# Kernel tuning notes

Measured on AMD Instinct MI355X. Metric: run time of the kernel, lower is better.

The kernel has to match this reference:

```python
import jax, jax.numpy as jnp
import numpy as np
import math

B, T, C = 32, 256, 1024
LAYER_ID, NUM_LAYERS = 12, 24
NEG_INF = -1e38


def setup_inputs() -> dict:
    key = jax.random.key(0)
    ks = jax.random.split(key, 5)
    x = jax.random.normal(ks[0], (B, T, C), dtype=jnp.float32)
    # deterministic parameter init, faithful to the torch __init__
    r01 = LAYER_ID / (NUM_LAYERS - 1)          # ratio_0_to_1
    r10 = 1.0 - LAYER_ID / NUM_LAYERS          # ratio_1_to_almost0
    h = jnp.arange(C, dtype=jnp.float32)
    time_decay = -5.0 + 8.0 * (h / (C - 1)) ** (0.7 + 1.3 * r01)
    tf = (jnp.arange(C) + 1) % 3 - 1
    time_first = jnp.full((C,), math.log(0.3), jnp.float32) + 0.5 * tf.astype(jnp.float32)
    xr = (jnp.arange(C, dtype=jnp.float32) / C)[None, None, :]   # [1,1,C]
    time_mix_k = xr ** r10
    time_mix_v = xr ** r10 + 0.3 * r01
    time_mix_r = xr ** (0.5 * r10)
    s = 1.0 / math.sqrt(C)
    Wk = jax.random.normal(ks[1], (C, C), jnp.float32) * s
    Wv = jax.random.normal(ks[2], (C, C), jnp.float32) * s
    Wr = jax.random.normal(ks[3], (C, C), jnp.float32) * s
    Wo = jax.random.normal(ks[4], (C, C), jnp.float32) * s
    return {"x": x, "time_decay": time_decay, "time_first": time_first,
            "time_mix_k": time_mix_k, "time_mix_v": time_mix_v, "time_mix_r": time_mix_r,
            "Wk": Wk, "Wv": Wv, "Wr": Wr, "Wo": Wo}


def wkv(time_decay, time_first, k, v):
    """Numerically-stabilized WKV scan. k,v: [B,T,C]; decay/first: [C]."""
    w = -jnp.exp(time_decay)   # per-channel log-decay (negative)
    u = time_first
    kT = jnp.swapaxes(k, 0, 1)  # [T,B,C]
    vT = jnp.swapaxes(v, 0, 1)

    def step(carry, kv):
        p, q, o = carry                       # p,q: running num/den; o: log scale
        kt, vt = kv                           # [B,C]
        no = jnp.maximum(o, u + kt)
        A = jnp.exp(o - no)
        Bc = jnp.exp(u + kt - no)
        y = (A * p + Bc * vt) / (A * q + Bc)
        no2 = jnp.maximum(w + o, kt)
        A2 = jnp.exp(w + o - no2)
        B2 = jnp.exp(kt - no2)
        return (A2 * p + B2 * vt, A2 * q + B2, no2), y

    init = (jnp.zeros((k.shape[0], k.shape[2]), k.dtype),
            jnp.zeros((k.shape[0], k.shape[2]), k.dtype),
            jnp.full((k.shape[0], k.shape[2]), NEG_INF, k.dtype))
    _, yT = jax.lax.scan(step, init, (kT, vT))
    return jnp.swapaxes(yT, 0, 1)  # [B,T,C]


def reference(x, time_decay, time_first, time_mix_k, time_mix_v, time_mix_r, Wk, Wv, Wr, Wo):
    # time_shift: xx[t] = x[t-1], xx[0] = 0
    xx = jnp.pad(x, ((0, 0), (1, 0), (0, 0)))[:, :-1, :]
    xk = x * time_mix_k + xx * (1.0 - time_mix_k)
    xv = x * time_mix_v + xx * (1.0 - time_mix_v)
    xr = x * time_mix_r + xx * (1.0 - time_mix_r)
    k = jnp.einsum('btc,dc->btd', xk, Wk)
    v = jnp.einsum('btc,dc->btd', xv, Wv)
    r = jnp.einsum('btc,dc->btd', xr, Wr)
    sr = jax.nn.sigmoid(r)
    rwkv = sr * wkv(time_decay, time_first, k, v)
    return jnp.einsum('btc,dc->btd', rwkv, Wo)
```

## Files before the change

### kernel.cpp

```cpp
#include <hip/hip_runtime.h>

#define Bdim 32
#define Tdim 256
#define Cdim 1024
#define Mrows (Bdim * Tdim)

typedef unsigned short u16;
typedef unsigned int u32;
typedef __bf16 bf16x8 __attribute__((ext_vector_type(8)));
typedef float f32x4 __attribute__((ext_vector_type(4)));

__device__ __forceinline__ float bf2f(u32 u) {
    union { u32 i; float f; } v; v.i = u << 16; return v.f;
}
__device__ __forceinline__ u16 f2bf(float f) {
    union { float f; u32 i; } v; v.f = f;
    u32 u = v.i;
    return (u16)((u + 0x7fffu + ((u >> 16) & 1u)) >> 16);
}

__device__ __forceinline__ void gload16(const u16* g, u16* l) {
    __builtin_amdgcn_global_load_lds(
        (__attribute__((address_space(1))) const void*)g,
        (__attribute__((address_space(3))) void*)l, 16, 0, 0);
}

__global__ __launch_bounds__(256) void prep_fused(
    const float* __restrict__ x, const float* __restrict__ tmk,
    const float* __restrict__ tmv, const float* __restrict__ tmr,
    u16* __restrict__ xk, u16* __restrict__ xv, u16* __restrict__ xr,
    const float* __restrict__ w0, const float* __restrict__ w1,
    const float* __restrict__ w2, const float* __restrict__ w3,
    u16* __restrict__ o0, u16* __restrict__ o1,
    u16* __restrict__ o2, u16* __restrict__ o3)
{
    int bid = blockIdx.x;
    if (bid < 4096) {
        int tid = bid * 256 + threadIdx.x;
        int e = tid << 3;
        int c = e & (Cdim - 1);
        int t = (e >> 10) & (Tdim - 1);
        float xf[8], xxf[8], mk[8], mv[8], mr[8];
        *(float4*)(xf)     = *(const float4*)(x + e);
        *(float4*)(xf + 4) = *(const float4*)(x + e + 4);
        if (t != 0) {
            *(float4*)(xxf)     = *(const float4*)(x + e - Cdim);
            *(float4*)(xxf + 4) = *(const float4*)(x + e - Cdim + 4);
        } else {
#pragma unroll
            for (int j = 0; j < 8; j++) xxf[j] = 0.f;
        }
        *(float4*)(mk)     = *(const float4*)(tmk + c);
        *(float4*)(mk + 4) = *(const float4*)(tmk + c + 4);
        *(float4*)(mv)     = *(const float4*)(tmv + c);
        *(float4*)(mv + 4) = *(const float4*)(tmv + c + 4);
        *(float4*)(mr)     = *(const float4*)(tmr + c);
        *(float4*)(mr + 4) = *(const float4*)(tmr + c + 4);
        u16 ok[8], ov[8], orr[8];
#pragma unroll
        for (int j = 0; j < 8; j++) {
            float d = xf[j] - xxf[j];
            ok[j]  = f2bf(xxf[j] + d * mk[j]);
            ov[j]  = f2bf(xxf[j] + d * mv[j]);
            orr[j] = f2bf(xxf[j] + d * mr[j]);
        }
        *(uint4*)(xk + e) = *(const uint4*)ok;
        *(uint4*)(xv + e) = *(const uint4*)ov;
        *(uint4*)(xr + e) = *(const uint4*)orr;
    } else {
        int wb = bid - 4096;
        int m = wb >> 9;
        const float* src; u16* dst;
        switch (m) {
            case 0: src = w0; dst = o0; break;
            case 1: src = w1; dst = o1; break;
            case 2: src = w2; dst = o2; break;
            default: src = w3; dst = o3; break;
        }
        int i = (((wb & 511) << 8) + threadIdx.x) << 3;
        float a[8];
        *(float4*)(a)     = *(const float4*)(src + i);
        *(float4*)(a + 4) = *(const float4*)(src + i + 4);
        u16 o[8];
#pragma unroll
        for (int j = 0; j < 8; j++) o[j] = f2bf(a[j]);
        *(uint4*)(dst + i) = *(const uint4*)o;
    }
}

template <int BF16OUT>
__device__ __forceinline__ void gemm_body(
    const u16* __restrict__ A, const u16* __restrict__ Bw, void* __restrict__ Cout,
    u16* As0, u16* Bs0, u16* As1, u16* Bs1, int bm, int bn)
{
    const int K = Cdim, N = Cdim;
    const int tid = threadIdx.x;
    const int lane = tid & 63, wave = tid >> 6;
    const int wm = (wave & 1) << 6, wn = (wave >> 1) << 6;
    const int fr = lane & 15, quad = lane >> 4;

    const int srow = tid >> 2;
    const int skc = (tid & 3) << 3;
    const u16* ga = A + (size_t)(bm * 128 + srow) * K + skc;
    const u16* gb = Bw + (size_t)(bn * 128 + srow) * K + skc;
    u16* la0 = As0 + (wave << 9);
    u16* lb0 = Bs0 + (wave << 9);
    u16* la1 = As1 + (wave << 9);
    u16* lb1 = Bs1 + (wave << 9);
    const size_t gstep = (size_t)64 * K;

    f32x4 acc[4][4];
#pragma unroll
    for (int i = 0; i < 4; i++)
#pragma unroll
        for (int j = 0; j < 4; j++)
            acc[i][j] = (f32x4){0.f, 0.f, 0.f, 0.f};

    for (int k0 = 0; k0 < K; k0 += 64) {
        __syncthreads();
        gload16(ga, la0);
        gload16(ga + gstep, la0 + 2048);
        gload16(gb, lb0);
        gload16(gb + gstep, lb0 + 2048);
        gload16(ga + 32, la1);
        gload16(ga + 32 + gstep, la1 + 2048);
        gload16(gb + 32, lb1);
        gload16(gb + 32 + gstep, lb1 + 2048);
        ga += 64; gb += 64;
        __syncthreads();
#pragma unroll
        for (int h = 0; h < 2; h++) {
            const u16* Ah = h ? As1 : As0;
            const u16* Bh = h ? Bs1 : Bs0;
            bf16x8 af[4], bfr[4];
#pragma unroll
            for (int i = 0; i < 4; i++) {
                af[i]  = *(const bf16x8*)(Ah + (wm + i * 16 + fr) * 32 + quad * 8);
                bfr[i] = *(const bf16x8*)(Bh + (wn + i * 16 + fr) * 32 + quad * 8);
            }
#pragma unroll
            for (int i = 0; i < 4; i++)
#pragma unroll
                for (int j = 0; j < 4; j++)
                    acc[i][j] = __builtin_amdgcn_mfma_f32_16x16x32_bf16(
                        af[i], bfr[j], acc[i][j], 0, 0, 0);
        }
    }

    const int gr0 = bm * 128 + wm + quad * 4;
    const int gc0 = bn * 128 + wn + fr;
#pragma unroll
    for (int i = 0; i < 4; i++)
#pragma unroll
        for (int j = 0; j < 4; j++)
#pragma unroll
            for (int r = 0; r < 4; r++) {
                int gr = gr0 + i * 16 + r;
                int gc = gc0 + j * 16;
                float val = acc[i][j][r];
                if (BF16OUT)
                    ((u16*)Cout)[(size_t)gr * N + gc] = f2bf(val);
                else
                    ((float*)Cout)[(size_t)gr * N + gc] = val;
            }
}

__global__ __launch_bounds__(256) void gemm3_kernel(
    const u16* __restrict__ xk, const u16* __restrict__ xv, const u16* __restrict__ xr,
    const u16* __restrict__ wk, const u16* __restrict__ wv, const u16* __restrict__ wr,
    u16* __restrict__ ck, u16* __restrict__ cv, u16* __restrict__ cr)
{
    __shared__ u16 As0[128 * 32], Bs0[128 * 32], As1[128 * 32], Bs1[128 * 32];
    const u16* A; const u16* Bw; u16* Cout;
    switch (blockIdx.z) {
        case 0:  A = xk; Bw = wk; Cout = ck; break;
        case 1:  A = xv; Bw = wv; Cout = cv; break;
        default: A = xr; Bw = wr; Cout = cr; break;
    }
    int bx = blockIdx.x;
    gemm_body<1>(A, Bw, (void*)Cout, As0, Bs0, As1, Bs1, bx & 63, bx >> 6);
}

__global__ __launch_bounds__(256) void gemmo_kernel(
    const u16* __restrict__ A, const u16* __restrict__ Bw, float* __restrict__ Cout)
{
    __shared__ u16 As0[128 * 32], Bs0[128 * 32], As1[128 * 32], Bs1[128 * 32];
    int bx = blockIdx.x;
    gemm_body<0>(A, Bw, (void*)Cout, As0, Bs0, As1, Bs1, bx & 63, bx >> 6);
}

#define WTC 16

#define LOADCHUNK(KA, VA, RA, T0)                                        \
    _Pragma("unroll")                                                    \
    for (int s = 0; s < WTC; s++) {                                      \
        size_t idx = base + (size_t)((T0) + s) * Cdim;                   \
        KA[s] = kb[idx]; VA[s] = vb[idx]; RA[s] = rb[idx];               \
    }

#define COMPCHUNK(KA, VA, RA, T0)                                        \
    _Pragma("unroll")                                                    \
    for (int s = 0; s < WTC; s++) {                                      \
        float kt = bf2f(KA[s]);                                          \
        float vt = bf2f(VA[s]);                                          \
        float rt = bf2f(RA[s]);                                          \
        float uk = u + kt;                                               \
        float no = fmaxf(o, uk);                                         \
        float Ae = __expf(o - no);                                       \
        float Bc = __expf(uk - no);                                      \
        float num = Ae * p + Bc * vt;                                    \
        float den = Ae * q + Bc;                                         \
        float y = num * __builtin_amdgcn_rcpf(den);                      \
        float sr = __builtin_amdgcn_rcpf(1.f + __expf(-rt));             \
        rwkv[base + (size_t)((T0) + s) * Cdim] = f2bf(y * sr);           \
        float wo = w + o;                                                \
        float no2 = fmaxf(wo, kt);                                       \
        float A2 = __expf(wo - no2);                                     \
        float B2 = __expf(kt - no2);                                     \
        p = A2 * p + B2 * vt;                                            \
        q = A2 * q + B2;                                                 \
        o = no2;                                                         \
    }

__global__ __launch_bounds__(64) void wkv_kernel(
    const u16* __restrict__ kb, const u16* __restrict__ vb,
    const u16* __restrict__ rb, const float* __restrict__ td,
    const float* __restrict__ tfirst, u16* __restrict__ rwkv)
{
    int lane = threadIdx.x;
    int blk = blockIdx.x;
    int b = blk >> 4;
    int c = ((blk & 15) << 6) + lane;
    float w = -__expf(td[c]);
    float u = tfirst[c];
    const size_t base = (size_t)b * Tdim * Cdim + c;

    u32 kA[WTC], vA[WTC], rA[WTC];
    u32 kB[WTC], vB[WTC], rB[WTC];
    float p = 0.f, q = 0.f, o = -1e38f;

    LOADCHUNK(kA, vA, rA, 0)
    for (int t0 = 0; t0 < Tdim; t0 += 2 * WTC) {
        LOADCHUNK(kB, vB, rB, t0 + WTC)
        COMPCHUNK(kA, vA, rA, t0)
        if (t0 + 2 * WTC < Tdim) {
            LOADCHUNK(kA, vA, rA, t0 + 2 * WTC)
        }
        COMPCHUNK(kB, vB, rB, t0 + WTC)
    }
}

extern "C" void kernel_launch(void* const* d_in, const int* in_sizes, int n_in,
                              void* d_out, int out_size, void* d_ws, size_t ws_size,
                              hipStream_t stream) {
    (void)in_sizes; (void)n_in; (void)out_size; (void)ws_size;
    const float* x   = (const float*)d_in[0];
    const float* td  = (const float*)d_in[1];
    const float* tfi = (const float*)d_in[2];
    const float* tmk = (const float*)d_in[3];
    const float* tmv = (const float*)d_in[4];
    const float* tmr = (const float*)d_in[5];
    const float* Wk  = (const float*)d_in[6];
    const float* Wv  = (const float*)d_in[7];
    const float* Wr  = (const float*)d_in[8];
    const float* Wo  = (const float*)d_in[9];

    char* ws = (char*)d_ws;
    const size_t MiB = (size_t)1 << 20;
    u16* xk    = (u16*)(ws);
    u16* xv    = (u16*)(ws + 16 * MiB);
    u16* xr    = (u16*)(ws + 32 * MiB);
    u16* wkb   = (u16*)(ws + 48 * MiB);
    u16* wvb   = (u16*)(ws + 50 * MiB);
    u16* wrb   = (u16*)(ws + 52 * MiB);
    u16* wob   = (u16*)(ws + 54 * MiB);
    u16* kb    = (u16*)(ws + 56 * MiB);
    u16* vb    = (u16*)(ws + 72 * MiB);
    u16* rb    = (u16*)(ws + 88 * MiB);
    u16* rwkvb = (u16*)(ws);

    prep_fused<<<6144, 256, 0, stream>>>(x, tmk, tmv, tmr, xk, xv, xr,
                                         Wk, Wv, Wr, Wo, wkb, wvb, wrb, wob);

    gemm3_kernel<<<dim3(512, 1, 3), 256, 0, stream>>>(xk, xv, xr, wkb, wvb, wrb,
                                                      kb, vb, rb);

    wkv_kernel<<<512, 64, 0, stream>>>(kb, vb, rb, td, tfi, rwkvb);

    gemmo_kernel<<<512, 256, 0, stream>>>(rwkvb, wob, (float*)d_out);
}
```

Before: 229.0 us.

## Store GEMM tiles in fragment order and interleave two batch scans per WKV thread

The GEMM staging now maps each wave's global_load_lds to a 16-row by 32-column fragment block, so each MFMA operand becomes a contiguous lane*8 LDS read. This is meant to remove the strided row-major reads and the LDS bank conflicts they cause. The WKV kernel now has each thread run two independent recurrences (batches b and b+16) interleaved, with half the blocks and smaller chunks. That gives the serial exp/rcp dependency chain instruction-level parallelism, at the cost of fewer waves and more registers.

```diff
diff --git a/kernel.cpp b/kernel.cpp
--- a/kernel.cpp
+++ b/kernel.cpp
@@ -99,15 +99,15 @@
     const int wm = (wave & 1) << 6, wn = (wave >> 1) << 6;
     const int fr = lane & 15, quad = lane >> 4;
 
-    const int srow = tid >> 2;
-    const int skc = (tid & 3) << 3;
+    const int srow = ((wave & 1) << 6) + ((wave >> 1) << 4) + fr;
+    const int skc = quad << 3;
     const u16* ga = A + (size_t)(bm * 128 + srow) * K + skc;
     const u16* gb = Bw + (size_t)(bn * 128 + srow) * K + skc;
     u16* la0 = As0 + (wave << 9);
     u16* lb0 = Bs0 + (wave << 9);
     u16* la1 = As1 + (wave << 9);
     u16* lb1 = Bs1 + (wave << 9);
-    const size_t gstep = (size_t)64 * K;
+    const size_t gstep = (size_t)32 * K;
 
     f32x4 acc[4][4];
 #pragma unroll
@@ -115,6 +115,8 @@
 #pragma unroll
         for (int j = 0; j < 4; j++)
             acc[i][j] = (f32x4){0.f, 0.f, 0.f, 0.f};
+
+    const int hA = wave & 1, hB = wave >> 1;
 
     for (int k0 = 0; k0 < K; k0 += 64) {
         __syncthreads();
@@ -135,8 +137,8 @@
             bf16x8 af[4], bfr[4];
 #pragma unroll
             for (int i = 0; i < 4; i++) {
-                af[i]  = *(const bf16x8*)(Ah + (wm + i * 16 + fr) * 32 + quad * 8);
-                bfr[i] = *(const bf16x8*)(Bh + (wn + i * 16 + fr) * 32 + quad * 8);
+                af[i]  = *(const bf16x8*)(Ah + (((i << 1) + hA) << 9) + (lane << 3));
+                bfr[i] = *(const bf16x8*)(Bh + (((i << 1) + hB) << 9) + (lane << 3));
             }
 #pragma unroll
             for (int i = 0; i < 4; i++)
@@ -189,18 +191,18 @@
     gemm_body<0>(A, Bw, (void*)Cout, As0, Bs0, As1, Bs1, bx & 63, bx >> 6);
 }
 
-#define WTC 16
-
-#define LOADCHUNK(KA, VA, RA, T0)                                        \
+#define WT 8
+
+#define LOADCHUNK(KA, VA, RA, BASE, T0)                                  \
     _Pragma("unroll")                                                    \
-    for (int s = 0; s < WTC; s++) {                                      \
-        size_t idx = base + (size_t)((T0) + s) * Cdim;                   \
+    for (int s = 0; s < WT; s++) {                                       \
+        size_t idx = (BASE) + (size_t)((T0) + s) * Cdim;                 \
         KA[s] = kb[idx]; VA[s] = vb[idx]; RA[s] = rb[idx];               \
     }
 
-#define COMPCHUNK(KA, VA, RA, T0)                                        \
+#define COMPCHUNK(KA, VA, RA, BASE, T0, p, q, o)                         \
     _Pragma("unroll")                                                    \
-    for (int s = 0; s < WTC; s++) {                                      \
+    for (int s = 0; s < WT; s++) {                                       \
         float kt = bf2f(KA[s]);                                          \
         float vt = bf2f(VA[s]);                                          \
         float rt = bf2f(RA[s]);                                          \
@@ -212,7 +214,7 @@
         float den = Ae * q + Bc;                                         \
         float y = num * __builtin_amdgcn_rcpf(den);                      \
         float sr = __builtin_amdgcn_rcpf(1.f + __expf(-rt));             \
-        rwkv[base + (size_t)((T0) + s) * Cdim] = f2bf(y * sr);           \
+        rwkv[(BASE) + (size_t)((T0) + s) * Cdim] = f2bf(y * sr);         \
         float wo = w + o;                                                \
         float no2 = fmaxf(wo, kt);                                       \
         float A2 = __expf(wo - no2);                                     \
@@ -229,24 +231,31 @@
 {
     int lane = threadIdx.x;
     int blk = blockIdx.x;
-    int b = blk >> 4;
+    int b0 = blk >> 4;
     int c = ((blk & 15) << 6) + lane;
     float w = -__expf(td[c]);
     float u = tfirst[c];
-    const size_t base = (size_t)b * Tdim * Cdim + c;
-
-    u32 kA[WTC], vA[WTC], rA[WTC];
-    u32 kB[WTC], vB[WTC], rB[WTC];
-    float p = 0.f, q = 0.f, o = -1e38f;
-
-    LOADCHUNK(kA, vA, rA, 0)
-    for (int t0 = 0; t0 < Tdim; t0 += 2 * WTC) {
-        LOADCHUNK(kB, vB, rB, t0 + WTC)
-        COMPCHUNK(kA, vA, rA, t0)
-        if (t0 + 2 * WTC < Tdim) {
-            LOADCHUNK(kA, vA, rA, t0 + 2 * WTC)
-        }
-        COMPCHUNK(kB, vB, rB, t0 + WTC)
+    const size_t base0 = (size_t)b0 * Tdim * Cdim + c;
+    const size_t base1 = (size_t)(b0 + 16) * Tdim * Cdim + c;
+
+    u32 k0A[WT], v0A[WT], r0A[WT], k0B[WT], v0B[WT], r0B[WT];
+    u32 k1A[WT], v1A[WT], r1A[WT], k1B[WT], v1B[WT], r1B[WT];
+    float p0 = 0.f, q0 = 0.f, o0 = -1e38f;
+    float p1 = 0.f, q1 = 0.f, o1 = -1e38f;
+
+    LOADCHUNK(k0A, v0A, r0A, base0, 0)
+    LOADCHUNK(k1A, v1A, r1A, base1, 0)
+    for (int t0 = 0; t0 < Tdim; t0 += 2 * WT) {
+        LOADCHUNK(k0B, v0B, r0B, base0, t0 + WT)
+        LOADCHUNK(k1B, v1B, r1B, base1, t0 + WT)
+        COMPCHUNK(k0A, v0A, r0A, base0, t0, p0, q0, o0)
+        COMPCHUNK(k1A, v1A, r1A, base1, t0, p1, q1, o1)
+        if (t0 + 2 * WT < Tdim) {
+            LOADCHUNK(k0A, v0A, r0A, base0, t0 + 2 * WT)
+            LOADCHUNK(k1A, v1A, r1A, base1, t0 + 2 * WT)
+        }
+        COMPCHUNK(k0B, v0B, r0B, base0, t0 + WT, p0, q0, o0)
+        COMPCHUNK(k1B, v1B, r1B, base1, t0 + WT, p1, q1, o1)
     }
 }
 
@@ -285,7 +294,7 @@
     gemm3_kernel<<<dim3(512, 1, 3), 256, 0, stream>>>(xk, xv, xr, wkb, wvb, wrb,
                                                       kb, vb, rb);
 
-    wkv_kernel<<<512, 64, 0, stream>>>(kb, vb, rb, td, tfi, rwkvb);
+    wkv_kernel<<<256, 64, 0, stream>>>(kb, vb, rb, td, tfi, rwkvb);
 
     gemmo_kernel<<<512, 256, 0, stream>>>(rwkvb, wob, (float*)d_out);
 }
```

New measurement: 301.2 us. 1.32x slower.
